# Kernel optimization log

Hardware: AMD Instinct MI355X
Metric: run time of the kernel (lower is better)

The kernel has to match this reference:

```python
import jax, jax.numpy as jnp
from jax import lax
import numpy as np

S = 1024      # number of superpoints (all valid, 60 pts each >= min_points)
P = 60        # points per superpoint (labels are contiguous blocks)
K = 10        # sample_k FPS representatives
NM = 800      # total number of SAM masks
H = W = 256   # mask image dims
FD = 512      # point feature dim (clip_dim)
SAMPLE_K = 10
RADIUS = 0.2
MASK_THRES = 0.2
SIM_THRES = 0.5
N_MASK = 5
TOP_K = 10


def setup_inputs() -> dict:
    key = jax.random.key(0)
    ks = jax.random.split(key, 8)
    centers = jax.random.normal(ks[0], (S, 3), jnp.float32)
    # tight clusters around centers so the radius-0.2 graph has edges
    pcds = (centers[:, None, :] + 0.03 * jax.random.normal(ks[1], (S, P, 3), jnp.float32)).reshape(S * P, 3)
    spt_labels = jnp.repeat(jnp.arange(S, dtype=jnp.int32), P)
    masks = jax.random.bernoulli(ks[2], 0.05, (NM, H, W))
    y = jax.random.randint(ks[3], (S * P,), 0, H, jnp.int32)
    x = jax.random.randint(ks[4], (S * P,), 0, W, jnp.int32)
    vis = jax.random.bernoulli(ks[5], 0.7, (S * P,)).astype(jnp.int32)
    mapping = jnp.stack([jnp.zeros(S * P, jnp.int32), y, x, vis], axis=1)
    sam_scores = jax.random.uniform(ks[6], (NM,), jnp.float32, 0.5, 1.0)
    point_feas = jax.random.normal(ks[7], (S * P, FD), jnp.float32)
    return {"pcds": pcds, "spt_labels": spt_labels, "masks": masks,
            "mapping": mapping, "sam_scores": sam_scores, "point_feas": point_feas}


def _fps_idx(pts, k):
    # pts: [P,3]. Deterministic start at index 0 (torch version uses a random start).
    d0 = jnp.sum((pts - pts[0]) ** 2, axis=1)
    def step(dist, _):
        idx = jnp.argmax(dist)
        nd = jnp.sum((pts - pts[idx]) ** 2, axis=1)
        return jnp.minimum(dist, nd), idx
    _, rest = lax.scan(step, d0, None, length=k - 1)
    return jnp.concatenate([jnp.zeros((1,), rest.dtype), rest])


def _forward(pcds, sam_scores, point_feas, spt_labels, masks, mapping):
    N = pcds.shape[0]
    pts_g = pcds.reshape(S, P, 3)  # labels are contiguous blocks of size P
    idxs = jax.vmap(lambda p: _fps_idx(lax.stop_gradient(p), SAMPLE_K))(pts_g)      # [S,K]
    reps = jnp.take_along_axis(pts_g, idxs[:, :, None], axis=1)                     # [S,K,3]

    # pairwise min distance between superpoint representative sets
    flat = reps.reshape(S * K, 3)
    sq = jnp.sum(flat ** 2, axis=1)
    d2 = jnp.maximum(sq[:, None] + sq[None, :] - 2.0 * (flat @ flat.T), 0.0)
    d = jnp.sqrt(d2 + 1e-12)
    mind = d.reshape(S, K, S, K).min(axis=(1, 3))                                   # [S,S]
    eye = jnp.eye(S, dtype=bool)
    adj0 = jnp.where((mind < RADIUS) & ~eye, jnp.exp(-mind), 0.0)

    # mask coverage per point, aggregated per superpoint
    vis = mapping[:, 3] == 1
    yy = jnp.clip(mapping[:, 1], 0, H - 1)
    xx = jnp.clip(mapping[:, 2], 0, W - 1)
    coverage = (masks[:, yy, xx].T & vis[:, None]).astype(jnp.float32)              # [N,NM]
    counts = jax.ops.segment_sum(jnp.ones((N,), jnp.float32), spt_labels, num_segments=S)[:, None]
    cov_g = jax.ops.segment_sum(coverage, spt_labels, num_segments=S)               # [S,NM]
    frac = cov_g / (counts + 1e-6)

    # per-mask keep only top_k superpoints by coverage fraction
    _, tki = lax.top_k(frac.T, TOP_K)                                               # [NM,TOP_K]
    tkm = jnp.zeros((NM, S), bool).at[jnp.arange(NM)[:, None], tki].set(True).T      # [S,NM]
    frac = jnp.where(tkm, frac, 0.0)
    contrib = frac >= MASK_THRES                                                     # [S,NM] bool

    # mean point features per superpoint, L2-normalized
    feats = jax.ops.segment_sum(point_feas, spt_labels, num_segments=S) / (counts + 1e-6)
    feats = feats / jnp.maximum(jnp.linalg.norm(feats, axis=1, keepdims=True), 1e-12)

    def row_mod(i):
        mi = contrib[i]                                                              # [NM]
        union = (mi[None, :] | contrib).astype(jnp.float32)                          # [S,NM]
        _, tk = lax.top_k(union, N_MASK)                                             # [S,N_MASK]
        ti = jnp.take_along_axis(jnp.broadcast_to(mi[None, :], (S, NM)), tk, axis=1)
        tj = jnp.take_along_axis(contrib, tk, axis=1)
        inter = (ti & tj).sum(1).astype(jnp.float32)
        uni = (ti | tj).sum(1).astype(jnp.float32)
        ov = inter / (uni + 1e-6)
        sim = jnp.clip((feats @ feats[i] + 1.0) * 0.5, 0.0, 1.0)
        sim = jnp.where(sim < SIM_THRES, 1.0, sim)
        return ov * sim

    mod = lax.map(row_mod, jnp.arange(S))                                            # [S,S], symmetric
    adjacency = jnp.where(adj0 > 0, jnp.maximum(mod, adj0), 0.0)

    weights = frac * sam_scores[None, :]
    conf = jnp.clip(weights.sum(1) / (frac.sum(1) + 1e-6), 0.0, None)
    return adjacency, conf


def reference(pcds, spt_labels, masks, mapping, sam_scores, point_feas):
    return _forward(pcds, sam_scores, point_feas, spt_labels, masks, mapping)
```

## Files before the change

kernel.cpp:

```cpp
#include <hip/hip_runtime.h>
#include <hip/hip_bf16.h>

#define SNUM 1024
#define PNUM 60
#define KFPS 10
#define NMASK 800
#define WORDS 25
#define HWDIM 256
#define FD 512
#define NPTS (SNUM*PNUM)
#define EDGE_CAP (1u<<20)

__device__ __forceinline__ float fmul(float a, float b){ return __fmul_rn(a,b); }
__device__ __forceinline__ float fadd(float a, float b){ return __fadd_rn(a,b); }
__device__ __forceinline__ float fsub(float a, float b){ return __fsub_rn(a,b); }

__device__ __forceinline__ float dist2f(float ax,float ay,float az,float bx,float by,float bz){
    float dx=fsub(ax,bx), dy=fsub(ay,by), dz=fsub(az,bz);
    return fadd(fadd(fmul(dx,dx),fmul(dy,dy)),fmul(dz,dz));
}

__global__ __launch_bounds__(64) void k_fps(const float* __restrict__ pcds,
                                            float* __restrict__ reps){
    int s = blockIdx.x;
    int l = threadIdx.x;
    float x=0.f,y=0.f,z=0.f;
    if (l < PNUM){
        const float* p = pcds + (size_t)(s*PNUM + l)*3;
        x=p[0]; y=p[1]; z=p[2];
    }
    float x0=__shfl(x,0), y0=__shfl(y,0), z0=__shfl(z,0);
    float dist = dist2f(x,y,z,x0,y0,z0);
    int sel[KFPS];
    sel[0]=0;
    #pragma unroll
    for(int it=1; it<KFPS; ++it){
        float v = (l<PNUM)? dist : -INFINITY;
        int idx = l;
        #pragma unroll
        for(int off=32; off; off>>=1){
            float ov = __shfl_xor(v, off);
            int   oi = __shfl_xor(idx, off);
            if (ov > v || (ov==v && oi<idx)){ v=ov; idx=oi; }
        }
        sel[it]=idx;
        float sx=__shfl(x,idx), sy=__shfl(y,idx), sz=__shfl(z,idx);
        float nd = dist2f(x,y,z,sx,sy,sz);
        dist = fminf(dist, nd);
    }
    #pragma unroll
    for(int j=0;j<KFPS;++j){
        float rx=__shfl(x,sel[j]), ry=__shfl(y,sel[j]), rz=__shfl(z,sel[j]);
        if (l==0){
            float* o = reps + (size_t)(s*KFPS+j)*3;
            o[0]=rx; o[1]=ry; o[2]=rz;
        }
    }
}

__global__ void k_detect(const unsigned char* __restrict__ m8, unsigned int* __restrict__ flag){
    int t = blockIdx.x*blockDim.x + threadIdx.x;
    for (int i = t; i < 65536; i += blockDim.x*gridDim.x){
        if ((i & 3) != 0 && m8[i] == 1) atomicOr(flag, 1u);
    }
}

__global__ __launch_bounds__(256) void k_pack(const unsigned char* __restrict__ m8,
                                              const int* __restrict__ m32,
                                              const unsigned int* __restrict__ flag,
                                              unsigned int* __restrict__ pb){
    __shared__ unsigned int lds[256*WORDS];
    int t = threadIdx.x;
    int pixBase = blockIdx.x * 256;
    int pixel = pixBase + t;
    if (*flag){
        for (int w=0; w<WORDS; ++w){
            unsigned int word = 0;
            #pragma unroll
            for (int b=0;b<32;++b)
                word |= (unsigned int)(m8[(size_t)((w*32+b))*65536 + pixel] & 1u) << b;
            lds[t*WORDS + w] = word;
        }
    } else {
        for (int w=0; w<WORDS; ++w){
            unsigned int word = 0;
            #pragma unroll
            for (int b=0;b<32;++b)
                word |= (unsigned int)(m32[(size_t)((w*32+b))*65536 + pixel] & 1) << b;
            lds[t*WORDS + w] = word;
        }
    }
    __syncthreads();
    uint4* out4 = (uint4*)(pb + (size_t)pixBase*WORDS);
    const uint4* l4 = (const uint4*)lds;
    for (int u=t; u<1600; u+=256) out4[u] = l4[u];
}

__global__ __launch_bounds__(256) void k_cov(const int* __restrict__ mapping,
                                             const unsigned int* __restrict__ pb,
                                             unsigned char* __restrict__ cntT){
    __shared__ int pxl[8][PNUM];
    int t = threadIdx.x;
    int sBase = blockIdx.x * 8;
    for (int idx=t; idx<8*PNUM; idx+=256){
        int ls = idx / PNUM, p = idx - ls*PNUM;
        const int4 v = ((const int4*)mapping)[(sBase+ls)*PNUM + p];
        int y = min(max(v.y,0),HWDIM-1), x = min(max(v.z,0),HWDIM-1);
        pxl[ls][p] = (v.w==1) ? ((y<<8)|x) : -1;
    }
    __syncthreads();
    int ls = t >> 5, w = t & 31;
    if (w >= WORDS) return;
    unsigned int acc8[8];
    #pragma unroll
    for (int k=0;k<8;++k) acc8[k]=0;
    #pragma unroll 6
    for (int p=0;p<PNUM;++p){
        int px = pxl[ls][p];
        if (px >= 0){
            unsigned int word = pb[(size_t)px*WORDS + w];
            #pragma unroll
            for (int k=0;k<8;++k)
                acc8[k] += (word >> k) & 0x01010101u;
        }
    }
    int s = sBase + ls;
    #pragma unroll
    for (int k=0;k<8;++k)
        #pragma unroll
        for (int j=0;j<4;++j){
            int b = k + 8*j;
            cntT[(size_t)(w*32+b)*SNUM + s] = (unsigned char)((acc8[k] >> (8*j)) & 0xFF);
        }
}

__global__ __launch_bounds__(256) void k_topk(const unsigned char* __restrict__ cntT,
                                              const float* __restrict__ scores,
                                              unsigned int* __restrict__ contrib,
                                              float* __restrict__ wsum,
                                              float* __restrict__ fsum){
    int m = blockIdx.x;
    int t = threadIdx.x;
    __shared__ int hist[64];
    __shared__ int scan_s[256];
    __shared__ int sT, sR;
    if (t < 64) hist[t]=0;
    __syncthreads();
    uchar4 c4 = ((const uchar4*)(cntT + (size_t)m*SNUM))[t];
    int c[4] = {(int)c4.x,(int)c4.y,(int)c4.z,(int)c4.w};
    atomicAdd(&hist[c[0]],1); atomicAdd(&hist[c[1]],1);
    atomicAdd(&hist[c[2]],1); atomicAdd(&hist[c[3]],1);
    __syncthreads();
    if (t==0){
        int running=0, T=0, r=10;
        for(int v=63;v>=0;--v){
            int nr = running + hist[v];
            if (nr >= 10){ T=v; r=10-running; break; }
            running = nr;
        }
        sT=T; sR=r;
    }
    __syncthreads();
    int T=sT, r=sR;
    int eq = (c[0]==T)+(c[1]==T)+(c[2]==T)+(c[3]==T);
    scan_s[t]=eq; __syncthreads();
    for(int off=1;off<256;off<<=1){
        int v = (t>=off)? scan_s[t-off] : 0;
        __syncthreads();
        scan_s[t]+=v;
        __syncthreads();
    }
    int rank = scan_s[t]-eq;
    float sc = scores[m];
    #pragma unroll
    for(int j=0;j<4;++j){
        int s = t*4+j;
        bool selv = (c[j]>T) || (c[j]==T && rank<r);
        if (c[j]==T) rank++;
        if (selv && c[j]>0){
            float frac = (float)c[j]/60.0f;
            atomicAdd(&wsum[s], frac*sc);
            atomicAdd(&fsum[s], frac);
            if (c[j] >= 12)
                atomicOr(&contrib[s*WORDS + (m>>5)], 1u<<(m&31));
        }
    }
}

__global__ __launch_bounds__(256) void k_adj0(const float* __restrict__ reps,
                                              float* __restrict__ out,
                                              unsigned int* __restrict__ ecnt,
                                              unsigned int* __restrict__ edges,
                                              const float* __restrict__ wsum,
                                              const float* __restrict__ fsum,
                                              float* __restrict__ conf){
    __shared__ float ri[16][KFPS][3], rj[16][KFPS][3];
    __shared__ float sqi[16][KFPS], sqj[16][KFPS];
    int tx = threadIdx.x, ty = threadIdx.y;
    int t = ty*16+tx;
    if (blockIdx.y==0 && blockIdx.x<4){
        int s = blockIdx.x*256 + t;
        conf[s] = fmaxf(wsum[s]/(fsum[s]+1e-6f), 0.0f);
    }
    int i0 = blockIdx.y*16, j0 = blockIdx.x*16;
    for(int u=t; u<16*KFPS*3; u+=256){
        ((float*)ri)[u] = reps[(size_t)i0*KFPS*3 + u];
        ((float*)rj)[u] = reps[(size_t)j0*KFPS*3 + u];
    }
    __syncthreads();
    if (t < 16*KFPS){
        int sp=t/KFPS, k=t%KFPS;
        float x=ri[sp][k][0], y=ri[sp][k][1], z=ri[sp][k][2];
        sqi[sp][k]=fadd(fadd(fmul(x,x),fmul(y,y)),fmul(z,z));
        x=rj[sp][k][0]; y=rj[sp][k][1]; z=rj[sp][k][2];
        sqj[sp][k]=fadd(fadd(fmul(x,x),fmul(y,y)),fmul(z,z));
    }
    __syncthreads();
    int i = i0+ty, j = j0+tx;
    float m2 = INFINITY;
    #pragma unroll 2
    for(int k=0;k<KFPS;++k){
        float ax=ri[ty][k][0], ay=ri[ty][k][1], az=ri[ty][k][2], as=sqi[ty][k];
        #pragma unroll
        for(int l=0;l<KFPS;++l){
            float dot = fadd(fadd(fmul(ax,rj[tx][l][0]),fmul(ay,rj[tx][l][1])),fmul(az,rj[tx][l][2]));
            float d2 = fmaxf(fsub(fadd(as,sqj[tx][l]), fmul(2.0f,dot)), 0.0f);
            m2 = fminf(m2,d2);
        }
    }
    float d = sqrtf(fadd(m2,1e-12f));
    bool edge = (d < 0.2f) && (i!=j);
    out[(size_t)i*SNUM + j] = edge ? expf(-d) : 0.0f;
    if (edge){
        unsigned int e = atomicAdd(ecnt, 1u);
        if (e < EDGE_CAP) edges[e] = ((unsigned int)i<<10) | (unsigned int)j;
    }
}

__global__ __launch_bounds__(256) void k_feats(const float* __restrict__ pf,
                                               float* __restrict__ feats){
    int s = blockIdx.x, t = threadIdx.x;
    int g = t >> 7;
    int c = t & 127;
    const float4* pf4 = (const float4*)pf;
    float4 a = make_float4(0.f,0.f,0.f,0.f);
    for (int p=g; p<PNUM; p+=2){
        float4 v = pf4[(size_t)(s*PNUM+p)*128 + c];
        a.x+=v.x; a.y+=v.y; a.z+=v.z; a.w+=v.w;
    }
    __shared__ float4 part[2][128];
    part[g][c] = a;
    __shared__ float red[256];
    __syncthreads();
    float4 m = make_float4(0.f,0.f,0.f,0.f);
    float ss = 0.f;
    if (g==0){
        float4 b = part[1][c];
        m.x=(a.x+b.x)/60.0f; m.y=(a.y+b.y)/60.0f; m.z=(a.z+b.z)/60.0f; m.w=(a.w+b.w)/60.0f;
        ss = m.x*m.x + m.y*m.y + m.z*m.z + m.w*m.w;
    }
    red[t] = ss; __syncthreads();
    for (int off=128; off; off>>=1){ if (t<off) red[t]+=red[t+off]; __syncthreads(); }
    float denom = fmaxf(sqrtf(red[0]), 1e-12f);
    if (g==0){
        float4 o; o.x=m.x/denom; o.y=m.y/denom; o.z=m.z/denom; o.w=m.w/denom;
        ((float4*)feats)[(size_t)s*128 + c] = o;
    }
}

__global__ __launch_bounds__(64) void k_mod(const unsigned int* __restrict__ ecnt,
                                            const unsigned int* __restrict__ edges,
                                            const unsigned int* __restrict__ contrib,
                                            const float* __restrict__ feats,
                                            float* __restrict__ out){
    unsigned int n = *ecnt; if (n > EDGE_CAP) n = EDGE_CAP;
    int lane = threadIdx.x;
    for (unsigned int e = blockIdx.x; e < n; e += gridDim.x){
        unsigned int pk = edges[e];
        int i = (int)(pk>>10), j = (int)(pk & 1023u);
        const float4* fi = (const float4*)(feats + (size_t)i*FD);
        const float4* fj = (const float4*)(feats + (size_t)j*FD);
        float dot = 0.f;
        #pragma unroll
        for(int r=0;r<2;++r){
            float4 a = fi[lane + 64*r], b = fj[lane + 64*r];
            dot += a.x*b.x + a.y*b.y + a.z*b.z + a.w*b.w;
        }
        #pragma unroll
        for(int off=32;off;off>>=1) dot += __shfl_xor(dot,off);

        unsigned int u=0, aw=0; int cw=0;
        if (lane < WORDS){
            unsigned int bi = contrib[i*WORDS+lane], bj = contrib[j*WORDS+lane];
            u = bi|bj; aw = bi&bj; cw = __popc(u);
        }
        int pre=0, ctot=0;
        for(int k2=0;k2<WORDS;++k2){
            int v=__shfl(cw,k2);
            ctot += v;
            if (k2<lane) pre += v;
        }
        int il=0;
        if (lane<WORDS && pre<5){
            unsigned int x=u;
            int lim = 5-pre;
            #pragma unroll
            for(int q=0;q<5;++q){
                if (q<lim && x){
                    int b = __ffs(x)-1;
                    il += (int)((aw>>b)&1u);
                    x &= x-1;
                }
            }
        }
        #pragma unroll
        for(int off=32;off;off>>=1) il += __shfl_xor(il,off);
        int uni = min(ctot,5);
        float ov = (float)il / ((float)uni + 1e-6f);
        float sim = fminf(fmaxf((dot+1.0f)*0.5f,0.0f),1.0f);
        if (sim < 0.5f) sim = 1.0f;
        float mod = ov*sim;
        if (lane==0){
            size_t o = (size_t)i*SNUM+j;
            out[o] = fmaxf(out[o], mod);
        }
    }
}

extern "C" void kernel_launch(void* const* d_in, const int* in_sizes, int n_in,
                              void* d_out, int out_size, void* d_ws, size_t ws_size,
                              hipStream_t stream){
    const float*         pcds    = (const float*)d_in[0];
    const unsigned char* masks8  = (const unsigned char*)d_in[2];
    const int*           masks32 = (const int*)d_in[2];
    const int*           mapping = (const int*)d_in[3];
    const float*         scores  = (const float*)d_in[4];
    const float*         pf      = (const float*)d_in[5];
    float* out_adj  = (float*)d_out;
    float* out_conf = out_adj + (size_t)SNUM*SNUM;

    char* ws = (char*)d_ws;
    float*         reps    = (float*)(ws + 0);
    unsigned int*  pb      = (unsigned int*)(ws + 368640);
    unsigned char* cntT    = (unsigned char*)(ws + 6922240);
    unsigned int*  contrib = (unsigned int*)(ws + 7741440);
    float*         wsum    = (float*)(ws + 7843840);
    float*         fsum    = (float*)(ws + 7847936);
    unsigned int*  ecnt    = (unsigned int*)(ws + 7852032);
    unsigned int*  dflag   = (unsigned int*)(ws + 7852036);
    unsigned int*  edges   = (unsigned int*)(ws + 7852288);
    float*         feats   = (float*)(ws + 12046592);

    hipMemsetAsync(ws + 7741440, 0, 110848, stream);

    k_detect<<<64, 256, 0, stream>>>(masks8, dflag);
    k_fps   <<<SNUM, 64, 0, stream>>>(pcds, reps);
    k_pack  <<<HWDIM*HWDIM/256, 256, 0, stream>>>(masks8, masks32, dflag, pb);
    k_cov   <<<SNUM/8, 256, 0, stream>>>(mapping, pb, cntT);
    k_topk  <<<NMASK, 256, 0, stream>>>(cntT, scores, contrib, wsum, fsum);
    k_adj0  <<<dim3(64,64), dim3(16,16), 0, stream>>>(reps, out_adj, ecnt, edges, wsum, fsum, out_conf);
    k_feats <<<SNUM, 256, 0, stream>>>(pf, feats);
    k_mod   <<<1024, 64, 0, stream>>>(ecnt, edges, contrib, feats, out_adj);
}
```

Measured before the change: 466.3 us.

## Vectorize mask packing, fold memset and detect into FPS, skip unused feats

```diff
diff --git a/kernel.cpp b/kernel.cpp
--- a/kernel.cpp
+++ b/kernel.cpp
@@ -20,10 +20,26 @@
     return fadd(fadd(fmul(dx,dx),fmul(dy,dy)),fmul(dz,dz));
 }
 
-__global__ __launch_bounds__(64) void k_fps(const float* __restrict__ pcds,
-                                            float* __restrict__ reps){
+__global__ __launch_bounds__(64) void k_initfps(const float* __restrict__ pcds,
+                                                float* __restrict__ reps,
+                                                unsigned int* __restrict__ zbase,
+                                                const unsigned char* __restrict__ m8,
+                                                unsigned int* __restrict__ dflag){
     int s = blockIdx.x;
     int l = threadIdx.x;
+    if (s < 64){
+        int tid = s*64 + l;
+        #pragma unroll
+        for (int k=0;k<8;++k){
+            int wi = tid + k*4096;
+            if (wi < 28673) zbase[wi] = 0u;
+        }
+        #pragma unroll
+        for (int k=0;k<16;++k){
+            int i = tid*16 + k;
+            if ((i & 3) != 0 && m8[i] == 1){ atomicOr(dflag, 1u); break; }
+        }
+    }
     float x=0.f,y=0.f,z=0.f;
     if (l < PNUM){
         const float* p = pcds + (size_t)(s*PNUM + l)*3;
@@ -55,13 +71,6 @@
             float* o = reps + (size_t)(s*KFPS+j)*3;
             o[0]=rx; o[1]=ry; o[2]=rz;
         }
-    }
-}
-
-__global__ void k_detect(const unsigned char* __restrict__ m8, unsigned int* __restrict__ flag){
-    int t = blockIdx.x*blockDim.x + threadIdx.x;
-    for (int i = t; i < 65536; i += blockDim.x*gridDim.x){
-        if ((i & 3) != 0 && m8[i] == 1) atomicOr(flag, 1u);
     }
 }
 
@@ -71,23 +80,35 @@
                                               unsigned int* __restrict__ pb){
     __shared__ unsigned int lds[256*WORDS];
     int t = threadIdx.x;
+    int wv = t >> 6, lane = t & 63;
     int pixBase = blockIdx.x * 256;
-    int pixel = pixBase + t;
-    if (*flag){
-        for (int w=0; w<WORDS; ++w){
-            unsigned int word = 0;
+    if (*flag & 1u){
+        const unsigned int* base32 = (const unsigned int*)m8;
+        int pix4 = (pixBase >> 2) + lane;
+        for (int w=wv; w<WORDS; w+=4){
+            unsigned int w0=0,w1=0,w2=0,w3=0;
             #pragma unroll
-            for (int b=0;b<32;++b)
-                word |= (unsigned int)(m8[(size_t)((w*32+b))*65536 + pixel] & 1u) << b;
-            lds[t*WORDS + w] = word;
+            for (int b=0;b<32;++b){
+                unsigned int u = base32[(size_t)(w*32+b)*16384 + pix4];
+                w0 |= (u & 1u) << b;
+                w1 |= ((u >> 8) & 1u) << b;
+                w2 |= ((u >> 16) & 1u) << b;
+                w3 |= ((u >> 24) & 1u) << b;
+            }
+            int p4 = lane*4;
+            lds[(p4+0)*WORDS+w]=w0; lds[(p4+1)*WORDS+w]=w1;
+            lds[(p4+2)*WORDS+w]=w2; lds[(p4+3)*WORDS+w]=w3;
         }
     } else {
-        for (int w=0; w<WORDS; ++w){
-            unsigned int word = 0;
-            #pragma unroll
-            for (int b=0;b<32;++b)
-                word |= (unsigned int)(m32[(size_t)((w*32+b))*65536 + pixel] & 1) << b;
-            lds[t*WORDS + w] = word;
+        for (int w=wv; w<WORDS; w+=4){
+            for (int i=0;i<4;++i){
+                int pixel = pixBase + lane*4 + i;
+                unsigned int word = 0;
+                #pragma unroll
+                for (int b=0;b<32;++b)
+                    word |= (unsigned int)(m32[(size_t)(w*32+b)*65536 + pixel] & 1) << b;
+                lds[(lane*4+i)*WORDS+w] = word;
+            }
         }
     }
     __syncthreads();
@@ -191,6 +212,7 @@
                                               float* __restrict__ out,
                                               unsigned int* __restrict__ ecnt,
                                               unsigned int* __restrict__ edges,
+                                              unsigned int* __restrict__ needed,
                                               const float* __restrict__ wsum,
                                               const float* __restrict__ fsum,
                                               float* __restrict__ conf){
@@ -234,12 +256,16 @@
     if (edge){
         unsigned int e = atomicAdd(ecnt, 1u);
         if (e < EDGE_CAP) edges[e] = ((unsigned int)i<<10) | (unsigned int)j;
+        atomicOr(&needed[i], 1u);
+        atomicOr(&needed[j], 1u);
     }
 }
 
 __global__ __launch_bounds__(256) void k_feats(const float* __restrict__ pf,
+                                               const unsigned int* __restrict__ needed,
                                                float* __restrict__ feats){
     int s = blockIdx.x, t = threadIdx.x;
+    if (!needed[s]) return;
     int g = t >> 7;
     int c = t & 127;
     const float4* pf4 = (const float4*)pf;
@@ -341,24 +367,23 @@
 
     char* ws = (char*)d_ws;
     float*         reps    = (float*)(ws + 0);
-    unsigned int*  pb      = (unsigned int*)(ws + 368640);
-    unsigned char* cntT    = (unsigned char*)(ws + 6922240);
-    unsigned int*  contrib = (unsigned int*)(ws + 7741440);
-    float*         wsum    = (float*)(ws + 7843840);
-    float*         fsum    = (float*)(ws + 7847936);
-    unsigned int*  ecnt    = (unsigned int*)(ws + 7852032);
-    unsigned int*  dflag   = (unsigned int*)(ws + 7852036);
-    unsigned int*  edges   = (unsigned int*)(ws + 7852288);
-    float*         feats   = (float*)(ws + 12046592);
-
-    hipMemsetAsync(ws + 7741440, 0, 110848, stream);
-
-    k_detect<<<64, 256, 0, stream>>>(masks8, dflag);
-    k_fps   <<<SNUM, 64, 0, stream>>>(pcds, reps);
-    k_pack  <<<HWDIM*HWDIM/256, 256, 0, stream>>>(masks8, masks32, dflag, pb);
-    k_cov   <<<SNUM/8, 256, 0, stream>>>(mapping, pb, cntT);
-    k_topk  <<<NMASK, 256, 0, stream>>>(cntT, scores, contrib, wsum, fsum);
-    k_adj0  <<<dim3(64,64), dim3(16,16), 0, stream>>>(reps, out_adj, ecnt, edges, wsum, fsum, out_conf);
-    k_feats <<<SNUM, 256, 0, stream>>>(pf, feats);
-    k_mod   <<<1024, 64, 0, stream>>>(ecnt, edges, contrib, feats, out_adj);
-}
+    unsigned int*  pb      = (unsigned int*)(ws + 131072);
+    unsigned char* cntT    = (unsigned char*)(ws + 6684672);
+    unsigned int*  contrib = (unsigned int*)(ws + 7503872);
+    float*         wsum    = (float*)(ws + 7606272);
+    float*         fsum    = (float*)(ws + 7610368);
+    unsigned int*  needed  = (unsigned int*)(ws + 7614464);
+    unsigned int*  ecnt    = (unsigned int*)(ws + 7618560);
+    unsigned int*  dflag   = (unsigned int*)(ws + 7618564);
+    unsigned int*  edges   = (unsigned int*)(ws + 7618568);
+    float*         feats   = (float*)(ws + 11812880);
+    unsigned int*  zbase   = (unsigned int*)(ws + 7503872);
+
+    k_initfps<<<SNUM, 64, 0, stream>>>(pcds, reps, zbase, masks8, dflag);
+    k_pack   <<<HWDIM*HWDIM/256, 256, 0, stream>>>(masks8, masks32, dflag, pb);
+    k_cov    <<<SNUM/8, 256, 0, stream>>>(mapping, pb, cntT);
+    k_topk   <<<NMASK, 256, 0, stream>>>(cntT, scores, contrib, wsum, fsum);
+    k_adj0   <<<dim3(64,64), dim3(16,16), 0, stream>>>(reps, out_adj, ecnt, edges, needed, wsum, fsum, out_conf);
+    k_feats  <<<SNUM, 256, 0, stream>>>(pf, needed, feats);
+    k_mod    <<<1024, 64, 0, stream>>>(ecnt, edges, contrib, feats, out_adj);
+}
```

Result: no change. 462.6 us (-0.8%).
